# Optimization experiments

Measured on AMD Instinct MI355X. Metric: run time of the kernel, lower is better.

The kernel has to match this reference:

```python
import jax, jax.numpy as jnp
import numpy as np

DIM = 1024
NUM_EXPERTS = 8
TOP_K = 2
HIDDEN = int(DIM * 4.0 * 2 / 3)  # 2730, matches GatedMLP hidden_dim
AUX_COEF = 0.01


def setup_inputs() -> dict:
    key = jax.random.key(0)
    ks = jax.random.split(key, 5)
    B, N = 4, 2048
    x = jax.random.normal(ks[0], (B, N, DIM), dtype=jnp.float32)
    # nn.Linear weights are [out, in]; y = x @ W.T
    gate_w = jax.random.normal(ks[1], (NUM_EXPERTS, DIM), dtype=jnp.float32) * 0.02
    w1 = jax.random.normal(ks[2], (NUM_EXPERTS, HIDDEN, DIM), dtype=jnp.float32) * 0.02
    w2 = jax.random.normal(ks[3], (NUM_EXPERTS, DIM, HIDDEN), dtype=jnp.float32) * 0.02
    w3 = jax.random.normal(ks[4], (NUM_EXPERTS, HIDDEN, DIM), dtype=jnp.float32) * 0.02
    return {"x": x, "gate_w": gate_w, "w1": w1, "w2": w2, "w3": w3}


def reference(x, gate_w, w1, w2, w3):
    # Router
    logits = jnp.einsum('bnd,ed->bne', x, gate_w)            # [B,N,E]
    probs = jax.nn.softmax(logits, axis=-1)                   # [B,N,E]
    top_v, top_i = jax.lax.top_k(probs, TOP_K)                # [B,N,K]
    top_v = top_v / jnp.sum(top_v, axis=-1, keepdims=True)
    # Combine weights per expert: sum_k prob_k * 1[idx_k == e]  -> [B,N,E]
    one_hot = jax.nn.one_hot(top_i, NUM_EXPERTS, dtype=x.dtype)  # [B,N,K,E]
    combine = jnp.einsum('bnk,bnke->bne', top_v, one_hot)
    # Per-expert SwiGLU MLP (dropout is identity in eval)
    out = jnp.zeros_like(x)
    for e in range(NUM_EXPERTS):
        h = jax.nn.silu(jnp.einsum('bnd,hd->bnh', x, w1[e])) \
            * jnp.einsum('bnd,hd->bnh', x, w3[e])             # [B,N,H]
        y = jnp.einsum('bnh,dh->bnd', h, w2[e])               # [B,N,D]
        out = out + combine[..., e:e + 1] * y
    # Load-balancing aux loss
    tokens_per_expert = jnp.mean(probs, axis=(0, 1))          # [E]
    uniform = 1.0 / NUM_EXPERTS
    aux_loss = AUX_COEF * jnp.mean((tokens_per_expert - uniform) ** 2)
    return out, aux_loss
```

## Files before the change

kernel.cpp:

```cpp
#include <hip/hip_runtime.h>
#include <hip/hip_bf16.h>
#include <stdint.h>

#define DIM   1024
#define NE    8
#define HID   2730
#define HPAD  2752
#define NTOK  8192
#define CAP   8192

typedef __bf16 bf16x8 __attribute__((ext_vector_type(8)));
typedef float  floatx4 __attribute__((ext_vector_type(4)));

__device__ __forceinline__ unsigned short f2bf(float f) {
    union { float f; unsigned int u; } v; v.f = f;
    unsigned int u = v.u;
    unsigned int r = (u + 0x7fffu + ((u >> 16) & 1u)) >> 16;
    return (unsigned short)r;
}

__device__ __forceinline__ void gl2lds16(const void* g, void* l) {
    __builtin_amdgcn_global_load_lds((const __attribute__((address_space(1))) void*)g,
                                     (__attribute__((address_space(3))) void*)l,
                                     16, 0, 0);
}

__global__ void convert_x_kernel(const float* __restrict__ x, unsigned short* __restrict__ xb) {
    int i = blockIdx.x * 256 + threadIdx.x;
    float4 v = ((const float4*)x)[i];
    uint2 o;
    o.x = (unsigned)f2bf(v.x) | ((unsigned)f2bf(v.y) << 16);
    o.y = (unsigned)f2bf(v.z) | ((unsigned)f2bf(v.w) << 16);
    *(uint2*)(xb + i * 4) = o;
}

__global__ void convert_w13_kernel(const float* __restrict__ w1, const float* __restrict__ w3,
                                   unsigned short* __restrict__ w1b, unsigned short* __restrict__ w3b) {
    const int HALF = (NE * HID * DIM) / 4;
    int i = blockIdx.x * 256 + threadIdx.x;
    const float* src; unsigned short* dst; int j;
    if (i < HALF) { src = w1; dst = w1b; j = i; }
    else          { src = w3; dst = w3b; j = i - HALF; }
    float4 v = ((const float4*)src)[j];
    uint2 o;
    o.x = (unsigned)f2bf(v.x) | ((unsigned)f2bf(v.y) << 16);
    o.y = (unsigned)f2bf(v.z) | ((unsigned)f2bf(v.w) << 16);
    *(uint2*)(dst + (size_t)j * 4) = o;
}

__global__ void convert_w2_kernel(const float* __restrict__ w2, unsigned short* __restrict__ w2b) {
    int i = blockIdx.x * 256 + threadIdx.x;
    int r = i / 688;
    int c = (i - r * 688) * 4;
    const float* src = w2 + r * HID;
    unsigned short q[4];
#pragma unroll
    for (int j = 0; j < 4; ++j) {
        int col = c + j;
        q[j] = (col < HID) ? f2bf(src[col]) : (unsigned short)0;
    }
    uint2 o;
    o.x = (unsigned)q[0] | ((unsigned)q[1] << 16);
    o.y = (unsigned)q[2] | ((unsigned)q[3] << 16);
    *(uint2*)(w2b + (size_t)r * HPAD + c) = o;
}

__global__ void router_kernel(const float* __restrict__ x, const float* __restrict__ gw,
                              int* __restrict__ toks, int* __restrict__ meta,
                              float* __restrict__ tokw,
                              int* __restrict__ counts, float* __restrict__ psum) {
    __shared__ float gws[NE * DIM];
    __shared__ float pblk[4][NE];
    int t = threadIdx.x;
    for (int i = t; i < NE * DIM; i += 256) gws[i] = gw[i];
    __syncthreads();

    int wv = t >> 6, lane = t & 63;
    int tok = blockIdx.x * 4 + wv;
    const float4* x4 = (const float4*)(x + (size_t)tok * DIM);

    float p[NE];
#pragma unroll
    for (int e = 0; e < NE; ++e) p[e] = 0.f;
#pragma unroll
    for (int c = 0; c < 4; ++c) {
        float4 xv = x4[c * 64 + lane];
#pragma unroll
        for (int e = 0; e < NE; ++e) {
            float4 gv = ((const float4*)(gws + e * DIM))[c * 64 + lane];
            p[e] += xv.x * gv.x + xv.y * gv.y + xv.z * gv.z + xv.w * gv.w;
        }
    }
#pragma unroll
    for (int e = 0; e < NE; ++e)
#pragma unroll
        for (int s = 32; s; s >>= 1) p[e] += __shfl_xor(p[e], s, 64);

    if (lane == 0) {
        float mx = p[0];
#pragma unroll
        for (int e = 1; e < NE; ++e) mx = fmaxf(mx, p[e]);
        float ex[NE], s = 0.f;
#pragma unroll
        for (int e = 0; e < NE; ++e) { ex[e] = __expf(p[e] - mx); s += ex[e]; }
        float inv = 1.f / s;
        int i1 = 0, i2 = 0; float v1 = -1.f, v2 = -1.f;
#pragma unroll
        for (int e = 0; e < NE; ++e) {
            float pe = ex[e] * inv;
            pblk[wv][e] = pe;
            if (pe > v1)      { v2 = v1; i2 = i1; v1 = pe; i1 = e; }
            else if (pe > v2) { v2 = pe; i2 = e; }
        }
        float wn = 1.f / (v1 + v2);
        int p1 = atomicAdd(&counts[i1], 1);
        toks[i1 * CAP + p1] = tok;
        meta[tok * 2]     = (i1 << 16) | p1;
        tokw[tok * 2]     = v1 * wn;
        int p2 = atomicAdd(&counts[i2], 1);
        toks[i2 * CAP + p2] = tok;
        meta[tok * 2 + 1] = (i2 << 16) | p2;
        tokw[tok * 2 + 1] = v2 * wn;
    }
    __syncthreads();
    if (t < NE) {
        float s = pblk[0][t] + pblk[1][t] + pblk[2][t] + pblk[3][t];
        atomicAdd(&psum[t], s);
    }
}

__global__ void finalize_kernel(const int* __restrict__ counts, int* __restrict__ offs,
                                const float* __restrict__ psum, float* __restrict__ aux_out) {
    if (threadIdx.x == 0) {
        int off = 0;
        for (int e = 0; e < NE; ++e) { offs[e] = off; off += counts[e]; }
        float s = 0.f;
        for (int e = 0; e < NE; ++e) {
            float d = psum[e] * (1.f / NTOK) - (1.f / NE);
            s += d * d;
        }
        aux_out[0] = 0.01f * s * (1.f / NE);
    }
}

__global__ __launch_bounds__(256, 2) void gemm1_kernel(
    const unsigned short* __restrict__ xb,
    const unsigned short* __restrict__ w1b,
    const unsigned short* __restrict__ w3b,
    unsigned short* __restrict__ h,
    const int* __restrict__ counts, const int* __restrict__ offs,
    const int* __restrict__ toks) {
    const int e = blockIdx.z;
    const int M = counts[e];
    const int m0 = blockIdx.y * 128;
    if (m0 >= M) return;
    const int n0 = blockIdx.x * 128;

    __shared__ unsigned short As[128 * 64];
    __shared__ unsigned short B1s[128 * 64];
    __shared__ unsigned short B3s[128 * 64];

    const int t = threadIdx.x;
    const int rb = t >> 3;
    const int kc = ((t & 7) ^ (rb & 7)) * 8;
    const int* tl = toks + e * CAP;
    int arow[4], brow[4];
#pragma unroll
    for (int i = 0; i < 4; ++i) {
        arow[i] = tl[min(m0 + rb + i * 32, M - 1)];
        brow[i] = min(n0 + rb + i * 32, HID - 1);
    }
    const unsigned short* w1e = w1b + (size_t)e * HID * DIM;
    const unsigned short* w3e = w3b + (size_t)e * HID * DIM;

    floatx4 acc1[4][4], acc3[4][4];
#pragma unroll
    for (int a = 0; a < 4; ++a)
#pragma unroll
        for (int b = 0; b < 4; ++b) {
            acc1[a][b] = (floatx4){0.f, 0.f, 0.f, 0.f};
            acc3[a][b] = (floatx4){0.f, 0.f, 0.f, 0.f};
        }

    const int wv = t >> 6, lane = t & 63;
    const int wm = (wv & 1) * 64, wn = (wv >> 1) * 64;
    const int lr = lane & 15, lq = lane >> 4;
    const int sw = lane & 7;

    for (int k0 = 0; k0 < DIM; k0 += 64) {
#pragma unroll
        for (int i = 0; i < 4; ++i) {
            const int ldso = (i * 256 + t) * 8;
            gl2lds16(xb + (size_t)arow[i] * DIM + k0 + kc, &As[ldso]);
            gl2lds16(w1e + (size_t)brow[i] * DIM + k0 + kc, &B1s[ldso]);
            gl2lds16(w3e + (size_t)brow[i] * DIM + k0 + kc, &B3s[ldso]);
        }
        __syncthreads();
#pragma unroll
        for (int kk = 0; kk < 64; kk += 32) {
            const int pc = (((kk >> 3) + lq) ^ sw) * 8;
            bf16x8 af[4];
#pragma unroll
            for (int mi = 0; mi < 4; ++mi)
                af[mi] = *(const bf16x8*)&As[(wm + mi * 16 + lr) * 64 + pc];
#pragma unroll
            for (int ni = 0; ni < 4; ++ni) {
                bf16x8 b1 = *(const bf16x8*)&B1s[(wn + ni * 16 + lr) * 64 + pc];
                bf16x8 b3 = *(const bf16x8*)&B3s[(wn + ni * 16 + lr) * 64 + pc];
#pragma unroll
                for (int mi = 0; mi < 4; ++mi) {
                    acc1[mi][ni] = __builtin_amdgcn_mfma_f32_16x16x32_bf16(af[mi], b1, acc1[mi][ni], 0, 0, 0);
                    acc3[mi][ni] = __builtin_amdgcn_mfma_f32_16x16x32_bf16(af[mi], b3, acc3[mi][ni], 0, 0, 0);
                }
            }
        }
        __syncthreads();
    }

    const int hb = offs[e];
#pragma unroll
    for (int mi = 0; mi < 4; ++mi) {
#pragma unroll
        for (int rg = 0; rg < 4; ++rg) {
            const int gm = m0 + wm + mi * 16 + lq * 4 + rg;
            if (gm >= M) continue;
            unsigned short* hrow = h + (size_t)(hb + gm) * HPAD;
#pragma unroll
            for (int ni = 0; ni < 4; ++ni) {
                const int col = n0 + wn + ni * 16 + lr;
                if (col >= HPAD) continue;
                float z1 = acc1[mi][ni][rg];
                float z3 = acc3[mi][ni][rg];
                float hv = z1 / (1.f + __expf(-z1)) * z3;
                hrow[col] = f2bf(hv);
            }
        }
    }
}

__global__ __launch_bounds__(256, 2) void gemm2_kernel(
    const unsigned short* __restrict__ h,
    const unsigned short* __restrict__ w2b,
    float* __restrict__ y,
    const int* __restrict__ counts, const int* __restrict__ offs) {
    const int e = blockIdx.z;
    const int M = counts[e];
    const int m0 = blockIdx.y * 128;
    if (m0 >= M) return;
    const int n0 = blockIdx.x * 128;

    __shared__ unsigned short As[128 * 64];
    __shared__ unsigned short Bs[128 * 64];

    const int t = threadIdx.x;
    const int rb = t >> 3;
    const int kc = ((t & 7) ^ (rb & 7)) * 8;
    const int hb = offs[e];
    int arow[4], brow[4];
#pragma unroll
    for (int i = 0; i < 4; ++i) {
        arow[i] = hb + min(m0 + rb + i * 32, M - 1);
        brow[i] = n0 + rb + i * 32;
    }
    const unsigned short* w2e = w2b + (size_t)e * DIM * HPAD;

    floatx4 acc[4][4];
#pragma unroll
    for (int a = 0; a < 4; ++a)
#pragma unroll
        for (int b = 0; b < 4; ++b) acc[a][b] = (floatx4){0.f, 0.f, 0.f, 0.f};

    const int wv = t >> 6, lane = t & 63;
    const int wm = (wv & 1) * 64, wn = (wv >> 1) * 64;
    const int lr = lane & 15, lq = lane >> 4;
    const int sw = lane & 7;

    for (int k0 = 0; k0 < HPAD; k0 += 64) {
#pragma unroll
        for (int i = 0; i < 4; ++i) {
            const int ldso = (i * 256 + t) * 8;
            gl2lds16(h + (size_t)arow[i] * HPAD + k0 + kc, &As[ldso]);
            gl2lds16(w2e + (size_t)brow[i] * HPAD + k0 + kc, &Bs[ldso]);
        }
        __syncthreads();
#pragma unroll
        for (int kk = 0; kk < 64; kk += 32) {
            const int pc = (((kk >> 3) + lq) ^ sw) * 8;
            bf16x8 af[4];
#pragma unroll
            for (int mi = 0; mi < 4; ++mi)
                af[mi] = *(const bf16x8*)&As[(wm + mi * 16 + lr) * 64 + pc];
#pragma unroll
            for (int ni = 0; ni < 4; ++ni) {
                bf16x8 bf = *(const bf16x8*)&Bs[(wn + ni * 16 + lr) * 64 + pc];
#pragma unroll
                for (int mi = 0; mi < 4; ++mi)
                    acc[mi][ni] = __builtin_amdgcn_mfma_f32_16x16x32_bf16(af[mi], bf, acc[mi][ni], 0, 0, 0);
            }
        }
        __syncthreads();
    }

#pragma unroll
    for (int mi = 0; mi < 4; ++mi) {
#pragma unroll
        for (int rg = 0; rg < 4; ++rg) {
            const int gm = m0 + wm + mi * 16 + lq * 4 + rg;
            if (gm >= M) continue;
            float* yrow = y + (size_t)(hb + gm) * DIM;
#pragma unroll
            for (int ni = 0; ni < 4; ++ni) {
                const int col = n0 + wn + ni * 16 + lr;
                yrow[col] = acc[mi][ni][rg];
            }
        }
    }
}

__global__ void combine_kernel(const float* __restrict__ y,
                               const int* __restrict__ meta,
                               const float* __restrict__ tokw,
                               const int* __restrict__ offs,
                               float* __restrict__ out) {
    const int tok = blockIdx.x;
    const int t = threadIdx.x;
    const int m0 = meta[tok * 2], m1 = meta[tok * 2 + 1];
    const float w0 = tokw[tok * 2], w1 = tokw[tok * 2 + 1];
    const int r0 = offs[m0 >> 16] + (m0 & 0xffff);
    const int r1 = offs[m1 >> 16] + (m1 & 0xffff);
    float4 a = ((const float4*)(y + (size_t)r0 * DIM))[t];
    float4 b = ((const float4*)(y + (size_t)r1 * DIM))[t];
    float4 o;
    o.x = w0 * a.x + w1 * b.x;
    o.y = w0 * a.y + w1 * b.y;
    o.z = w0 * a.z + w1 * b.z;
    o.w = w0 * a.w + w1 * b.w;
    ((float4*)(out + (size_t)tok * DIM))[t] = o;
}

extern "C" void kernel_launch(void* const* d_in, const int* in_sizes, int n_in,
                              void* d_out, int out_size, void* d_ws, size_t ws_size,
                              hipStream_t stream) {
    const float* x  = (const float*)d_in[0];
    const float* gw = (const float*)d_in[1];
    const float* w1 = (const float*)d_in[2];
    const float* w2 = (const float*)d_in[3];
    const float* w3 = (const float*)d_in[4];
    float* out = (float*)d_out;

    char* ws = (char*)d_ws;
    size_t o = 0;
    auto alloc = [&](size_t bytes) -> void* {
        void* p = ws + o;
        o += (bytes + 255) & ~(size_t)255;
        return p;
    };
    unsigned short* xb   = (unsigned short*)alloc((size_t)NTOK * DIM * 2);
    unsigned short* w1b  = (unsigned short*)alloc((size_t)NE * HID * DIM * 2);
    unsigned short* w3b  = (unsigned short*)alloc((size_t)NE * HID * DIM * 2);
    unsigned short* w2b  = (unsigned short*)alloc((size_t)NE * DIM * HPAD * 2);
    unsigned short* hbuf = (unsigned short*)alloc((size_t)2 * NTOK * HPAD * 2);
    int*   toks   = (int*)alloc((size_t)NE * CAP * 4);
    int*   meta   = (int*)alloc((size_t)NTOK * 2 * 4);
    float* tokw   = (float*)alloc((size_t)NTOK * 2 * 4);
    int*   counts = (int*)alloc(256);
    float* psum   = (float*)alloc(256);
    int*   offs   = (int*)alloc(256);
    if (o > ws_size) return;
    float* ybuf = (float*)w1b;

    hipMemsetAsync(counts, 0, 256, stream);
    hipMemsetAsync(psum, 0, 256, stream);

    convert_x_kernel<<<8192, 256, 0, stream>>>(x, xb);
    convert_w13_kernel<<<43680, 256, 0, stream>>>(w1, w3, w1b, w3b);
    convert_w2_kernel<<<22016, 256, 0, stream>>>(w2, w2b);
    router_kernel<<<2048, 256, 0, stream>>>(x, gw, toks, meta, tokw, counts, psum);
    finalize_kernel<<<1, 64, 0, stream>>>(counts, offs, psum, out + (size_t)NTOK * DIM);
    gemm1_kernel<<<dim3(22, 64, 8), 256, 0, stream>>>(xb, w1b, w3b, hbuf, counts, offs, toks);
    gemm2_kernel<<<dim3(8, 64, 8), 256, 0, stream>>>(hbuf, w2b, ybuf, counts, offs);
    combine_kernel<<<NTOK, 256, 0, stream>>>(ybuf, meta, tokw, offs, out);
}
```

Measured before the change: 899.6 us.

## Fuse conversions, split-K gemm2 with bf16 partials, reorder grid for M-fastest

Folds the x-to-bf16 conversion into the router kernel and merges the w1/w3 and w2 conversion kernels into one launch. The gemm1 and gemm2 grids are transposed so token tiles vary fastest, and gemm2 is split in two along K with each half writing bf16 partial results; the combine kernel then sums the two partials. Fewer launches and more gemm2 blocks should improve occupancy, and the bf16 partials halve the intermediate y traffic. The cost is lower precision for the partial sums, extra reads in combine, and reuse of the xb buffer for y, which assumes xb is no longer needed once gemm1 has run.

Result: slower. 1.056 ms (+17.4%).

```diff
diff --git a/kernel.cpp b/kernel.cpp
--- a/kernel.cpp
+++ b/kernel.cpp
@@ -8,6 +8,7 @@
 #define HPAD  2752
 #define NTOK  8192
 #define CAP   8192
+#define NSLOT 16384
 
 typedef __bf16 bf16x8 __attribute__((ext_vector_type(8)));
 typedef float  floatx4 __attribute__((ext_vector_type(4)));
@@ -19,53 +20,53 @@
     return (unsigned short)r;
 }
 
+__device__ __forceinline__ float bf2f(unsigned short b) {
+    union { unsigned int u; float f; } v; v.u = (unsigned int)b << 16;
+    return v.f;
+}
+
 __device__ __forceinline__ void gl2lds16(const void* g, void* l) {
     __builtin_amdgcn_global_load_lds((const __attribute__((address_space(1))) void*)g,
                                      (__attribute__((address_space(3))) void*)l,
                                      16, 0, 0);
 }
 
-__global__ void convert_x_kernel(const float* __restrict__ x, unsigned short* __restrict__ xb) {
-    int i = blockIdx.x * 256 + threadIdx.x;
-    float4 v = ((const float4*)x)[i];
-    uint2 o;
-    o.x = (unsigned)f2bf(v.x) | ((unsigned)f2bf(v.y) << 16);
-    o.y = (unsigned)f2bf(v.z) | ((unsigned)f2bf(v.w) << 16);
-    *(uint2*)(xb + i * 4) = o;
-}
-
-__global__ void convert_w13_kernel(const float* __restrict__ w1, const float* __restrict__ w3,
-                                   unsigned short* __restrict__ w1b, unsigned short* __restrict__ w3b) {
+__global__ void convert_w_kernel(const float* __restrict__ w1, const float* __restrict__ w3,
+                                 const float* __restrict__ w2,
+                                 unsigned short* __restrict__ w1b, unsigned short* __restrict__ w3b,
+                                 unsigned short* __restrict__ w2b) {
     const int HALF = (NE * HID * DIM) / 4;
-    int i = blockIdx.x * 256 + threadIdx.x;
-    const float* src; unsigned short* dst; int j;
-    if (i < HALF) { src = w1; dst = w1b; j = i; }
-    else          { src = w3; dst = w3b; j = i - HALF; }
-    float4 v = ((const float4*)src)[j];
-    uint2 o;
-    o.x = (unsigned)f2bf(v.x) | ((unsigned)f2bf(v.y) << 16);
-    o.y = (unsigned)f2bf(v.z) | ((unsigned)f2bf(v.w) << 16);
-    *(uint2*)(dst + (size_t)j * 4) = o;
-}
-
-__global__ void convert_w2_kernel(const float* __restrict__ w2, unsigned short* __restrict__ w2b) {
-    int i = blockIdx.x * 256 + threadIdx.x;
-    int r = i / 688;
-    int c = (i - r * 688) * 4;
-    const float* src = w2 + r * HID;
-    unsigned short q[4];
-#pragma unroll
-    for (int j = 0; j < 4; ++j) {
-        int col = c + j;
-        q[j] = (col < HID) ? f2bf(src[col]) : (unsigned short)0;
-    }
-    uint2 o;
-    o.x = (unsigned)q[0] | ((unsigned)q[1] << 16);
-    o.y = (unsigned)q[2] | ((unsigned)q[3] << 16);
-    *(uint2*)(w2b + (size_t)r * HPAD + c) = o;
+    const int W13  = 2 * HALF;
+    int gid = blockIdx.x * 256 + threadIdx.x;
+    if (gid < W13) {
+        const float* src; unsigned short* dst; int j;
+        if (gid < HALF) { src = w1; dst = w1b; j = gid; }
+        else            { src = w3; dst = w3b; j = gid - HALF; }
+        float4 v = ((const float4*)src)[j];
+        uint2 o;
+        o.x = (unsigned)f2bf(v.x) | ((unsigned)f2bf(v.y) << 16);
+        o.y = (unsigned)f2bf(v.z) | ((unsigned)f2bf(v.w) << 16);
+        *(uint2*)(dst + (size_t)j * 4) = o;
+    } else {
+        int i = gid - W13;
+        int r = i / 688;
+        int c = (i - r * 688) * 4;
+        const float* src = w2 + r * HID;
+        unsigned short q[4];
+#pragma unroll
+        for (int j = 0; j < 4; ++j) {
+            int col = c + j;
+            q[j] = (col < HID) ? f2bf(src[col]) : (unsigned short)0;
+        }
+        uint2 o;
+        o.x = (unsigned)q[0] | ((unsigned)q[1] << 16);
+        o.y = (unsigned)q[2] | ((unsigned)q[3] << 16);
+        *(uint2*)(w2b + (size_t)r * HPAD + c) = o;
+    }
 }
 
 __global__ void router_kernel(const float* __restrict__ x, const float* __restrict__ gw,
+                              unsigned short* __restrict__ xb,
                               int* __restrict__ toks, int* __restrict__ meta,
                               float* __restrict__ tokw,
                               int* __restrict__ counts, float* __restrict__ psum) {
@@ -78,6 +79,7 @@
     int wv = t >> 6, lane = t & 63;
     int tok = blockIdx.x * 4 + wv;
     const float4* x4 = (const float4*)(x + (size_t)tok * DIM);
+    uint2* xbrow = (uint2*)(xb + (size_t)tok * DIM);
 
     float p[NE];
 #pragma unroll
@@ -85,6 +87,10 @@
 #pragma unroll
     for (int c = 0; c < 4; ++c) {
         float4 xv = x4[c * 64 + lane];
+        uint2 o;
+        o.x = (unsigned)f2bf(xv.x) | ((unsigned)f2bf(xv.y) << 16);
+        o.y = (unsigned)f2bf(xv.z) | ((unsigned)f2bf(xv.w) << 16);
+        xbrow[c * 64 + lane] = o;
 #pragma unroll
         for (int e = 0; e < NE; ++e) {
             float4 gv = ((const float4*)(gws + e * DIM))[c * 64 + lane];
@@ -152,9 +158,9 @@
     const int* __restrict__ toks) {
     const int e = blockIdx.z;
     const int M = counts[e];
-    const int m0 = blockIdx.y * 128;
+    const int m0 = blockIdx.x * 128;
     if (m0 >= M) return;
-    const int n0 = blockIdx.x * 128;
+    const int n0 = blockIdx.y * 128;
 
     __shared__ unsigned short As[128 * 64];
     __shared__ unsigned short B1s[128 * 64];
@@ -241,13 +247,14 @@
 __global__ __launch_bounds__(256, 2) void gemm2_kernel(
     const unsigned short* __restrict__ h,
     const unsigned short* __restrict__ w2b,
-    float* __restrict__ y,
+    unsigned short* __restrict__ yh,
     const int* __restrict__ counts, const int* __restrict__ offs) {
-    const int e = blockIdx.z;
+    const int e  = blockIdx.z >> 1;
+    const int kh = blockIdx.z & 1;
     const int M = counts[e];
-    const int m0 = blockIdx.y * 128;
+    const int m0 = blockIdx.x * 128;
     if (m0 >= M) return;
-    const int n0 = blockIdx.x * 128;
+    const int n0 = blockIdx.y * 128;
 
     __shared__ unsigned short As[128 * 64];
     __shared__ unsigned short Bs[128 * 64];
@@ -275,7 +282,9 @@
     const int lr = lane & 15, lq = lane >> 4;
     const int sw = lane & 7;
 
-    for (int k0 = 0; k0 < HPAD; k0 += 64) {
+    const int kbeg = kh ? 22 * 64 : 0;
+    const int kend = kh ? HPAD : 22 * 64;
+    for (int k0 = kbeg; k0 < kend; k0 += 64) {
 #pragma unroll
         for (int i = 0; i < 4; ++i) {
             const int ldso = (i * 256 + t) * 8;
@@ -301,23 +310,24 @@
         __syncthreads();
     }
 
+    unsigned short* ybase = yh + (size_t)kh * NSLOT * DIM;
 #pragma unroll
     for (int mi = 0; mi < 4; ++mi) {
 #pragma unroll
         for (int rg = 0; rg < 4; ++rg) {
             const int gm = m0 + wm + mi * 16 + lq * 4 + rg;
             if (gm >= M) continue;
-            float* yrow = y + (size_t)(hb + gm) * DIM;
+            unsigned short* yrow = ybase + (size_t)(hb + gm) * DIM;
 #pragma unroll
             for (int ni = 0; ni < 4; ++ni) {
                 const int col = n0 + wn + ni * 16 + lr;
-                yrow[col] = acc[mi][ni][rg];
+                yrow[col] = f2bf(acc[mi][ni][rg]);
             }
         }
     }
 }
 
-__global__ void combine_kernel(const float* __restrict__ y,
+__global__ void combine_kernel(const unsigned short* __restrict__ yh,
                                const int* __restrict__ meta,
                                const float* __restrict__ tokw,
                                const int* __restrict__ offs,
@@ -326,15 +336,19 @@
     const int t = threadIdx.x;
     const int m0 = meta[tok * 2], m1 = meta[tok * 2 + 1];
     const float w0 = tokw[tok * 2], w1 = tokw[tok * 2 + 1];
-    const int r0 = offs[m0 >> 16] + (m0 & 0xffff);
-    const int r1 = offs[m1 >> 16] + (m1 & 0xffff);
-    float4 a = ((const float4*)(y + (size_t)r0 * DIM))[t];
-    float4 b = ((const float4*)(y + (size_t)r1 * DIM))[t];
+    const size_t r0 = (size_t)(offs[m0 >> 16] + (m0 & 0xffff)) * DIM;
+    const size_t r1 = (size_t)(offs[m1 >> 16] + (m1 & 0xffff)) * DIM;
+    const unsigned short* p0 = yh;
+    const unsigned short* p1 = yh + (size_t)NSLOT * DIM;
+    uint2 a0 = ((const uint2*)(p0 + r0))[t];
+    uint2 a1 = ((const uint2*)(p1 + r0))[t];
+    uint2 b0 = ((const uint2*)(p0 + r1))[t];
+    uint2 b1 = ((const uint2*)(p1 + r1))[t];
     float4 o;
-    o.x = w0 * a.x + w1 * b.x;
-    o.y = w0 * a.y + w1 * b.y;
-    o.z = w0 * a.z + w1 * b.z;
-    o.w = w0 * a.w + w1 * b.w;
+    o.x = w0 * (bf2f(a0.x & 0xffff) + bf2f(a1.x & 0xffff)) + w1 * (bf2f(b0.x & 0xffff) + bf2f(b1.x & 0xffff));
+    o.y = w0 * (bf2f(a0.x >> 16)    + bf2f(a1.x >> 16))    + w1 * (bf2f(b0.x >> 16)    + bf2f(b1.x >> 16));
+    o.z = w0 * (bf2f(a0.y & 0xffff) + bf2f(a1.y & 0xffff)) + w1 * (bf2f(b0.y & 0xffff) + bf2f(b1.y & 0xffff));
+    o.w = w0 * (bf2f(a0.y >> 16)    + bf2f(a1.y >> 16))    + w1 * (bf2f(b0.y >> 16)    + bf2f(b1.y >> 16));
     ((float4*)(out + (size_t)tok * DIM))[t] = o;
 }
 
@@ -359,7 +373,7 @@
     unsigned short* w1b  = (unsigned short*)alloc((size_t)NE * HID * DIM * 2);
     unsigned short* w3b  = (unsigned short*)alloc((size_t)NE * HID * DIM * 2);
     unsigned short* w2b  = (unsigned short*)alloc((size_t)NE * DIM * HPAD * 2);
-    unsigned short* hbuf = (unsigned short*)alloc((size_t)2 * NTOK * HPAD * 2);
+    unsigned short* hbuf = (unsigned short*)alloc((size_t)NSLOT * HPAD * 2);
     int*   toks   = (int*)alloc((size_t)NE * CAP * 4);
     int*   meta   = (int*)alloc((size_t)NTOK * 2 * 4);
     float* tokw   = (float*)alloc((size_t)NTOK * 2 * 4);
@@ -367,17 +381,15 @@
     float* psum   = (float*)alloc(256);
     int*   offs   = (int*)alloc(256);
     if (o > ws_size) return;
-    float* ybuf = (float*)w1b;
+    unsigned short* yh = (unsigned short*)xb;
 
     hipMemsetAsync(counts, 0, 256, stream);
     hipMemsetAsync(psum, 0, 256, stream);
 
-    convert_x_kernel<<<8192, 256, 0, stream>>>(x, xb);
-    convert_w13_kernel<<<43680, 256, 0, stream>>>(w1, w3, w1b, w3b);
-    convert_w2_kernel<<<22016, 256, 0, stream>>>(w2, w2b);
-    router_kernel<<<2048, 256, 0, stream>>>(x, gw, toks, meta, tokw, counts, psum);
+    router_kernel<<<2048, 256, 0, stream>>>(x, gw, xb, toks, meta, tokw, counts, psum);
     finalize_kernel<<<1, 64, 0, stream>>>(counts, offs, psum, out + (size_t)NTOK * DIM);
-    gemm1_kernel<<<dim3(22, 64, 8), 256, 0, stream>>>(xb, w1b, w3b, hbuf, counts, offs, toks);
-    gemm2_kernel<<<dim3(8, 64, 8), 256, 0, stream>>>(hbuf, w2b, ybuf, counts, offs);
-    combine_kernel<<<NTOK, 256, 0, stream>>>(ybuf, meta, tokw, offs, out);
-}
+    convert_w_kernel<<<65696, 256, 0, stream>>>(w1, w3, w2, w1b, w3b, w2b);
+    gemm1_kernel<<<dim3(64, 22, 8), 256, 0, stream>>>(xb, w1b, w3b, hbuf, counts, offs, toks);
+    gemm2_kernel<<<dim3(64, 8, 16), 256, 0, stream>>>(hbuf, w2b, yh, counts, offs);
+    combine_kernel<<<NTOK, 256, 0, stream>>>(yh, meta, tokw, offs, out);
+}
```
